# Optimization experiments

Measured on AMD Instinct MI355X. Metric: run time of the kernel, lower is better.

The kernel has to match this reference:

```python
import jax, jax.numpy as jnp
import numpy as np
import math

D_MODEL = 1024
N_HEAD = 16
D_HEAD = D_MODEL // N_HEAD


def setup_inputs() -> dict:
    key = jax.random.key(0)
    k0, k1, k2, k3, k4 = jax.random.split(key, 5)
    B, N = 4, 2048
    inp = jax.random.normal(k0, (B, N, D_MODEL), dtype=jnp.float32)
    # causal mask: True = keep (masked_fill on ~mask)
    mask = jnp.tril(jnp.ones((N, N), dtype=bool))
    # qkv_proj Linear(d_model, 3*d_model); output Linear(d_model, d_model)
    s_in = 1.0 / math.sqrt(D_MODEL)
    W_qkv = jax.random.uniform(k1, (D_MODEL, 3 * D_MODEL), jnp.float32, -s_in, s_in)
    b_qkv = jax.random.uniform(k2, (3 * D_MODEL,), jnp.float32, -s_in, s_in)
    W_out = jax.random.uniform(k3, (D_MODEL, D_MODEL), jnp.float32, -s_in, s_in)
    b_out = jax.random.uniform(k4, (D_MODEL,), jnp.float32, -s_in, s_in)
    return {"input": inp, "W_qkv": W_qkv, "b_qkv": b_qkv,
            "W_out": W_out, "b_out": b_out, "mask": mask}


def reference(input, W_qkv, b_qkv, W_out, b_out, mask):
    B, N, d = input.shape
    qkv = input @ W_qkv + b_qkv                       # [B,N,3d]  (dropout=eval no-op)
    q, k, v = jnp.split(qkv, 3, axis=-1)
    # [B,N,H,Dh] -> [B,H,N,Dh]
    q = q.reshape(B, N, N_HEAD, D_HEAD).transpose(0, 2, 1, 3)
    k = k.reshape(B, N, N_HEAD, D_HEAD).transpose(0, 2, 1, 3)
    v = v.reshape(B, N, N_HEAD, D_HEAD).transpose(0, 2, 1, 3)
    scale = 1.0 / math.sqrt(D_HEAD)
    scores = jnp.einsum('bhqd,bhkd->bhqk', q, k) * scale   # [B,H,N,N]
    scores = jnp.where(mask, scores, -jnp.inf)
    attn = jax.nn.softmax(scores, axis=-1)
    out = jnp.einsum('bhqk,bhkd->bhqd', attn, v)           # [B,H,N,Dh]
    out = out.transpose(0, 2, 1, 3).reshape(B, N, d)       # concat heads
    return out @ W_out + b_out
```

## Files before the change

kernel.cpp:

```cpp
#include <hip/hip_runtime.h>
#include <hip/hip_bf16.h>

typedef unsigned short u16;
typedef unsigned u32;
typedef __attribute__((ext_vector_type(4))) unsigned short u16x4;
typedef __attribute__((ext_vector_type(8))) unsigned short u16x8;
typedef __attribute__((ext_vector_type(4))) unsigned u32x4;
typedef __attribute__((ext_vector_type(8))) __bf16 bf16x8;
typedef __attribute__((ext_vector_type(4))) float f32x4;

typedef __attribute__((address_space(1))) void as1v;
typedef __attribute__((address_space(3))) void as3v;

#define MFMA16(a, b, c) __builtin_amdgcn_mfma_f32_16x16x32_bf16(a, b, c, 0, 0, 0)

__device__ __forceinline__ u16 f2bf(float f) {
    unsigned u = __builtin_bit_cast(unsigned, f);
    u += 0x7fffu + ((u >> 16) & 1u);
    return (u16)(u >> 16);
}

__device__ __forceinline__ u32 pkbf(float lo, float hi) {
    u32 r;
    asm("v_cvt_pk_bf16_f32 %0, %1, %2" : "=v"(r) : "v"(lo), "v"(hi));
    return r;
}

__device__ __forceinline__ void gload16(const void* g, void* l) {
    __builtin_amdgcn_global_load_lds((as1v*)g, (as3v*)l, 16, 0, 0);
}

__global__ void convert_f32_bf16(const float* __restrict__ in, u16* __restrict__ out, int n4) {
    int i = blockIdx.x * blockDim.x + threadIdx.x;
    if (i < n4) {
        float4 v = *(const float4*)&in[(size_t)i * 4];
        u16x4 o;
        o.x = f2bf(v.x); o.y = f2bf(v.y); o.z = f2bf(v.z); o.w = f2bf(v.w);
        *(u16x4*)&out[(size_t)i * 4] = o;
    }
}

__global__ void transpose_convert(const float* __restrict__ in, u16* __restrict__ out, int R, int C) {
    __shared__ float tl[64][65];
    const int rb = blockIdx.x, cb = blockIdx.y;
    const int tid = threadIdx.x;
    for (int it = 0; it < 4; ++it) {
        int lin = (tid + it * 256) * 4;
        int r = lin >> 6, c = lin & 63;
        float4 v = *(const float4*)&in[(size_t)(rb * 64 + r) * C + cb * 64 + c];
        tl[r][c + 0] = v.x; tl[r][c + 1] = v.y; tl[r][c + 2] = v.z; tl[r][c + 3] = v.w;
    }
    __syncthreads();
    for (int it = 0; it < 4; ++it) {
        int lin = (tid + it * 256) * 4;
        int oc = lin >> 6, orr = lin & 63;
        u16x4 o;
        o.x = f2bf(tl[orr + 0][oc]);
        o.y = f2bf(tl[orr + 1][oc]);
        o.z = f2bf(tl[orr + 2][oc]);
        o.w = f2bf(tl[orr + 3][oc]);
        *(u16x4*)&out[(size_t)(cb * 64 + oc) * R + rb * 64 + orr] = o;
    }
}

__global__ void transpose_v(const u16* __restrict__ vbuf, u16* __restrict__ vtb) {
    __shared__ u16 tl[64][65];
    const int nb = blockIdx.x, bh = blockIdx.y;
    const int tid = threadIdx.x;
    for (int it = 0; it < 2; ++it) {
        int lin = (tid + it * 256) * 8;
        int nl = lin >> 6, dh = lin & 63;
        u16x8 v = *(const u16x8*)&vbuf[((size_t)bh * 2048 + nb * 64 + nl) * 64 + dh];
#pragma unroll
        for (int j = 0; j < 8; ++j) tl[dh + j][nl] = v[j];
    }
    __syncthreads();
    for (int it = 0; it < 2; ++it) {
        int lin = (tid + it * 256) * 8;
        int dh = lin >> 6, nl = lin & 63;
        u16x8 o;
#pragma unroll
        for (int j = 0; j < 8; ++j) o[j] = tl[dh][nl + j];
        *(u16x8*)&vtb[((size_t)bh * 64 + dh) * 2048 + nb * 64 + nl] = o;
    }
}

__global__ __launch_bounds__(256) void gemm_bt(
    const u16* __restrict__ A, const u16* __restrict__ Bt, const float* __restrict__ bias,
    int M, int N, int K, int mode,
    u16* __restrict__ qb, u16* __restrict__ kb, u16* __restrict__ vb, float* __restrict__ outf) {
    __shared__ u16 Al[128 * 32];
    __shared__ u16 Bl[128 * 32];
    const int bm = blockIdx.x, bn = blockIdx.y;
    const int tid = threadIdx.x, wid = tid >> 6, lane = tid & 63;
    const int wr = wid >> 1, wc = wid & 1;
    const int l15 = lane & 15, lhi = lane >> 4;

    f32x4 acc[4][4];
#pragma unroll
    for (int i = 0; i < 4; ++i)
#pragma unroll
        for (int j = 0; j < 4; ++j) acc[i][j] = (f32x4){0.f, 0.f, 0.f, 0.f};

    for (int k0 = 0; k0 < K; k0 += 32) {
        __syncthreads();
#pragma unroll
        for (int s = 0; s < 2; ++s) {
            int lin0 = (wid * 2 + s) * 1024;
            int off = lin0 + lane * 16;
            int row = off >> 6, colb = off & 63;
            const u16* ga = A + (size_t)(bm * 128 + row) * K + k0 + (colb >> 1);
            gload16(ga, (char*)Al + lin0);
            const u16* gb = Bt + (size_t)(bn * 128 + row) * K + k0 + (colb >> 1);
            gload16(gb, (char*)Bl + lin0);
        }
        __syncthreads();
        bf16x8 af[4], bfr[4];
#pragma unroll
        for (int mt = 0; mt < 4; ++mt)
            af[mt] = *(const bf16x8*)&Al[(wr * 64 + mt * 16 + l15) * 32 + lhi * 8];
#pragma unroll
        for (int nt = 0; nt < 4; ++nt)
            bfr[nt] = *(const bf16x8*)&Bl[(wc * 64 + nt * 16 + l15) * 32 + lhi * 8];
#pragma unroll
        for (int mt = 0; mt < 4; ++mt)
#pragma unroll
            for (int nt = 0; nt < 4; ++nt)
                acc[mt][nt] = MFMA16(af[mt], bfr[nt], acc[mt][nt]);
    }

#pragma unroll
    for (int mt = 0; mt < 4; ++mt)
#pragma unroll
        for (int nt = 0; nt < 4; ++nt)
#pragma unroll
            for (int v = 0; v < 4; ++v) {
                int rg = bm * 128 + wr * 64 + mt * 16 + lhi * 4 + v;
                int cg = bn * 128 + wc * 64 + nt * 16 + l15;
                float val = acc[mt][nt][v] + bias[cg];
                if (mode == 0) {
                    int which = cg >> 10, rem = cg & 1023;
                    int hh = rem >> 6, dh = rem & 63;
                    int bb = rg >> 11, n = rg & 2047;
                    size_t idx = (((size_t)bb * 16 + hh) * 2048 + n) * 64 + dh;
                    if (which == 0) qb[idx] = f2bf(val * 0.18033688011112042f);
                    else if (which == 1) kb[idx] = f2bf(val);
                    else vb[idx] = f2bf(val);
                } else {
                    outf[(size_t)rg * N + cg] = val;
                }
            }
}

__global__ __launch_bounds__(256, 2) void attn_kernel(
    const u16* __restrict__ qbuf, const u16* __restrict__ kbuf,
    const u16* __restrict__ vtb, u16* __restrict__ obuf) {
    __shared__ u16 Kl[2][64 * 64];
    __shared__ u16 Vl[2][64 * 64];
    const int p = blockIdx.x, bh = blockIdx.y;
    const int b = bh >> 4, h = bh & 15;
    const int tid = threadIdx.x, wid = tid >> 6, lane = tid & 63;
    const int l15 = lane & 15, lhi = lane >> 4;
    const int qA0 = p * 64 + wid * 16;
    const int qB0 = (31 - p) * 64 + wid * 16;
    const int ntA = p + 1;
    const int ntmax = 32 - p;

    bf16x8 qfA[2], qfB[2];
    {
        const u16* qa = qbuf + ((size_t)bh * 2048 + qA0 + l15) * 64 + lhi * 8;
        const u16* qbp = qbuf + ((size_t)bh * 2048 + qB0 + l15) * 64 + lhi * 8;
        qfA[0] = *(const bf16x8*)(qa);
        qfA[1] = *(const bf16x8*)(qa + 32);
        qfB[0] = *(const bf16x8*)(qbp);
        qfB[1] = *(const bf16x8*)(qbp + 32);
    }

    float mA = -1e30f, lA = 0.f, mB = -1e30f, lB = 0.f;
    f32x4 oA[4], oB[4];
#pragma unroll
    for (int d = 0; d < 4; ++d) {
        oA[d] = (f32x4){0.f, 0.f, 0.f, 0.f};
        oB[d] = (f32x4){0.f, 0.f, 0.f, 0.f};
    }

    const int srow = lane >> 3;
    const int scolb = ((lane & 7) * 16) ^ (srow << 4);

    auto stage = [&](int buf, int t) {
        const int kbase = t * 64;
#pragma unroll
        for (int s = 0; s < 2; ++s) {
            int sg = wid * 2 + s;
            int row = sg * 8 + srow;
            const u16* gk = kbuf + ((size_t)bh * 2048 + kbase + row) * 64 + (scolb >> 1);
            gload16(gk, (char*)Kl[buf] + sg * 1024);
            const u16* gv = vtb + ((size_t)bh * 64 + row) * 2048 + kbase + (scolb >> 1);
            gload16(gv, (char*)Vl[buf] + sg * 1024);
        }
    };

    auto computeTile = [&](int bufc, int t, int q0, const bf16x8* qf,
                           float& m, float& l, f32x4* oa) {
        const char* Kb = (const char*)Kl[bufc];
        const char* Vb = (const char*)Vl[bufc];
        f32x4 s[4];
        __builtin_amdgcn_s_setprio(1);
#pragma unroll
        for (int kb4 = 0; kb4 < 4; ++kb4) {
            const int r = kb4 * 16 + l15;
            const int sw = (r & 7) << 4;
            const int rowb = r * 128;
            f32x4 a = (f32x4){0.f, 0.f, 0.f, 0.f};
            a = MFMA16(*(const bf16x8*)(Kb + rowb + ((lhi * 16) ^ sw)), qf[0], a);
            a = MFMA16(*(const bf16x8*)(Kb + rowb + ((64 + lhi * 16) ^ sw)), qf[1], a);
            s[kb4] = a;
        }
        __builtin_amdgcn_s_setprio(0);
        const int qg = q0 + l15;
        if (64 * t + 63 > q0) {
#pragma unroll
            for (int kb4 = 0; kb4 < 4; ++kb4)
#pragma unroll
                for (int v = 0; v < 4; ++v) {
                    int kg = 64 * t + kb4 * 16 + lhi * 4 + v;
                    if (kg > qg) s[kb4][v] = -1e30f;
                }
        }
        float pm = fmaxf(fmaxf(fmaxf(s[0][0], s[0][1]), fmaxf(s[0][2], s[0][3])),
                         fmaxf(fmaxf(s[1][0], s[1][1]), fmaxf(s[1][2], s[1][3])));
        pm = fmaxf(pm, fmaxf(fmaxf(fmaxf(s[2][0], s[2][1]), fmaxf(s[2][2], s[2][3])),
                             fmaxf(fmaxf(s[3][0], s[3][1]), fmaxf(s[3][2], s[3][3]))));
        pm = fmaxf(pm, __shfl_xor(pm, 16, 64));
        pm = fmaxf(pm, __shfl_xor(pm, 32, 64));
        float nm = fmaxf(m, pm);
        float f = exp2f(m - nm);
        m = nm;
        float rs = 0.f;
#pragma unroll
        for (int kb4 = 0; kb4 < 4; ++kb4)
#pragma unroll
            for (int v = 0; v < 4; ++v) {
                float e = exp2f(s[kb4][v] - nm);
                s[kb4][v] = e;
                rs += e;
            }
        rs += __shfl_xor(rs, 16, 64);
        rs += __shfl_xor(rs, 32, 64);
        l = l * f + rs;
#pragma unroll
        for (int d = 0; d < 4; ++d)
#pragma unroll
            for (int v = 0; v < 4; ++v) oa[d][v] *= f;
        u32 pw0[4], pw1[4];
        pw0[0] = pkbf(s[0][0], s[0][1]); pw0[1] = pkbf(s[0][2], s[0][3]);
        pw0[2] = pkbf(s[1][0], s[1][1]); pw0[3] = pkbf(s[1][2], s[1][3]);
        pw1[0] = pkbf(s[2][0], s[2][1]); pw1[1] = pkbf(s[2][2], s[2][3]);
        pw1[2] = pkbf(s[3][0], s[3][1]); pw1[3] = pkbf(s[3][2], s[3][3]);
        __builtin_amdgcn_s_setprio(1);
#pragma unroll
        for (int ks = 0; ks < 2; ++ks) {
            bf16x8 pb = __builtin_bit_cast(bf16x8,
                ks == 0 ? (u32x4){pw0[0], pw0[1], pw0[2], pw0[3]}
                        : (u32x4){pw1[0], pw1[1], pw1[2], pw1[3]});
#pragma unroll
            for (int dhb = 0; dhb < 4; ++dhb) {
                const int r = dhb * 16 + l15;
                const int sw = (r & 7) << 4;
                u16x4 v0 = *(const u16x4*)(Vb + r * 128 + ((ks * 64 + 8 * lhi) ^ sw));
                u16x4 v1 = *(const u16x4*)(Vb + r * 128 + ((ks * 64 + 32 + 8 * lhi) ^ sw));
                u16x8 vv = {v0[0], v0[1], v0[2], v0[3], v1[0], v1[1], v1[2], v1[3]};
                oa[dhb] = MFMA16(__builtin_bit_cast(bf16x8, vv), pb, oa[dhb]);
            }
        }
        __builtin_amdgcn_s_setprio(0);
    };

    stage(0, 0);
    int cur = 0;
    for (int t = 0; t < ntmax; ++t) {
        __syncthreads();
        if (t + 1 < ntmax) stage(cur ^ 1, t + 1);
        computeTile(cur, t, qB0, qfB, mB, lB, oB);
        if (t < ntA) computeTile(cur, t, qA0, qfA, mA, lA, oA);
        cur ^= 1;
    }

    auto epi = [&](int q0, float l, const f32x4* oa) {
        const float rl = 1.f / l;
        const int q = q0 + l15;
        const size_t rowoff = ((size_t)b * 2048 + q) * 1024 + h * 64;
#pragma unroll
        for (int dhb = 0; dhb < 4; ++dhb) {
            u16x4 w;
#pragma unroll
            for (int v = 0; v < 4; ++v) w[v] = f2bf(oa[dhb][v] * rl);
            *(u16x4*)&obuf[rowoff + dhb * 16 + lhi * 4] = w;
        }
    };
    epi(qA0, lA, oA);
    epi(qB0, lB, oB);
}

extern "C" void kernel_launch(void* const* d_in, const int* in_sizes, int n_in,
                              void* d_out, int out_size, void* d_ws, size_t ws_size,
                              hipStream_t stream) {
    const float* inp   = (const float*)d_in[0];
    const float* W_qkv = (const float*)d_in[1];
    const float* b_qkv = (const float*)d_in[2];
    const float* W_out = (const float*)d_in[3];
    const float* b_out = (const float*)d_in[4];
    float* out = (float*)d_out;

    u16* xb   = (u16*)d_ws;
    u16* wqt  = xb + 8388608;
    u16* wot  = wqt + 3145728;
    u16* qbuf = wot + 1048576;
    u16* kbuf = qbuf + 8388608;
    u16* vbuf = kbuf + 8388608;
    u16* vtb  = vbuf + 8388608;
    u16* obuf = vtb + 8388608;

    convert_f32_bf16<<<8192, 256, 0, stream>>>(inp, xb, 2097152);
    transpose_convert<<<dim3(16, 48), 256, 0, stream>>>(W_qkv, wqt, 1024, 3072);
    transpose_convert<<<dim3(16, 16), 256, 0, stream>>>(W_out, wot, 1024, 1024);
    gemm_bt<<<dim3(64, 24), 256, 0, stream>>>(xb, wqt, b_qkv, 8192, 3072, 1024, 0,
                                              qbuf, kbuf, vbuf, nullptr);
    transpose_v<<<dim3(32, 64), 256, 0, stream>>>(vbuf, vtb);
    attn_kernel<<<dim3(16, 64), 256, 0, stream>>>(qbuf, kbuf, vtb, obuf);
    gemm_bt<<<dim3(64, 8), 256, 0, stream>>>(obuf, wot, b_out, 8192, 1024, 1024, 1,
                                             nullptr, nullptr, nullptr, out);
}
```

Before: 219.1 us.

## Replace QKV projection GEMM with 256x256-tile pipelined kernel

New measurement: 206.5 us. 5.7% less time.

```diff
diff --git a/kernel.cpp b/kernel.cpp
--- a/kernel.cpp
+++ b/kernel.cpp
@@ -82,6 +82,132 @@
 #pragma unroll
         for (int j = 0; j < 8; ++j) o[j] = tl[dh][nl + j];
         *(u16x8*)&vtb[((size_t)bh * 64 + dh) * 2048 + nb * 64 + nl] = o;
+    }
+}
+
+__global__ __launch_bounds__(512, 2) void gemm256_qkv(
+    const u16* __restrict__ A, const u16* __restrict__ Bt, const float* __restrict__ bias,
+    u16* __restrict__ qb, u16* __restrict__ kb, u16* __restrict__ vb) {
+    constexpr int K = 1024;
+    constexpr int NT = 32;
+    __shared__ u16 ldsu[65536];
+
+    const int bid = blockIdx.x;
+    const int swz = (bid & 7) * 48 + (bid >> 3);
+    const int bm = swz / 12, bn = swz % 12;
+
+    const int tid = threadIdx.x, wid = tid >> 6, lane = tid & 63;
+    const int wr = wid >> 2, wc = wid & 3;
+    const int l15 = lane & 15, lhi = lane >> 4;
+
+    const int sslot = (lane & 7) ^ (lane >> 3);
+    const int kcol = (sslot & 3) * 8;
+    const int mloc = (lane >> 3) * 2 + (sslot >> 2);
+
+    const u16* Arow[2];
+    const u16* Brow[2];
+#pragma unroll
+    for (int li = 0; li < 2; ++li) {
+        int sg = wid * 2 + li;
+        int m = sg * 16 + mloc;
+        Arow[li] = A + (size_t)(bm * 256 + m) * K + kcol;
+        Brow[li] = Bt + (size_t)(bn * 256 + m) * K + kcol;
+    }
+
+    auto stageA = [&](int buf, int t) {
+#pragma unroll
+        for (int li = 0; li < 2; ++li) {
+            int sg = wid * 2 + li;
+            gload16(Arow[li] + t * 32, (char*)ldsu + buf * 32768 + sg * 1024);
+        }
+    };
+    auto stageB = [&](int buf, int t) {
+#pragma unroll
+        for (int li = 0; li < 2; ++li) {
+            int sg = wid * 2 + li;
+            gload16(Brow[li] + t * 32, (char*)ldsu + buf * 32768 + 16384 + sg * 1024);
+        }
+    };
+
+    const int rslot = ((l15 & 1) * 4 + lhi) ^ ((l15 >> 1) & 7);
+    const int fragoff = (l15 >> 1) * 64 + rslot * 8;
+
+    f32x4 acc[8][4];
+#pragma unroll
+    for (int i = 0; i < 8; ++i)
+#pragma unroll
+        for (int j = 0; j < 4; ++j) acc[i][j] = (f32x4){0.f, 0.f, 0.f, 0.f};
+
+    auto doTile = [&](int cur, int tstage, bool dostage) {
+        const u16* Ab = ldsu + cur * 16384 + wr * 4096 + fragoff;
+        const u16* Bb = ldsu + cur * 16384 + 8192 + wc * 2048 + fragoff;
+        bf16x8 af[8], b0, b1;
+#pragma unroll
+        for (int mf = 0; mf < 8; ++mf) af[mf] = *(const bf16x8*)(Ab + mf * 512);
+        b0 = *(const bf16x8*)(Bb);
+        b1 = *(const bf16x8*)(Bb + 512);
+        if (dostage) stageA(tstage & 3, tstage);
+        __builtin_amdgcn_s_setprio(1);
+#pragma unroll
+        for (int mf = 0; mf < 8; ++mf) {
+            acc[mf][0] = MFMA16(af[mf], b0, acc[mf][0]);
+            acc[mf][1] = MFMA16(af[mf], b1, acc[mf][1]);
+        }
+        __builtin_amdgcn_s_setprio(0);
+        b0 = *(const bf16x8*)(Bb + 1024);
+        b1 = *(const bf16x8*)(Bb + 1536);
+        if (dostage) stageB(tstage & 3, tstage);
+        __builtin_amdgcn_s_setprio(1);
+#pragma unroll
+        for (int mf = 0; mf < 8; ++mf) {
+            acc[mf][2] = MFMA16(af[mf], b0, acc[mf][2]);
+            acc[mf][3] = MFMA16(af[mf], b1, acc[mf][3]);
+        }
+        __builtin_amdgcn_s_setprio(0);
+    };
+
+    stageA(0, 0); stageB(0, 0);
+    stageA(1, 1); stageB(1, 1);
+    stageA(2, 2); stageB(2, 2);
+    asm volatile("s_waitcnt vmcnt(8)" ::: "memory");
+    __builtin_amdgcn_s_barrier();
+    __builtin_amdgcn_sched_barrier(0);
+
+    for (int t = 0; t < NT - 3; ++t) {
+        doTile(t & 3, t + 3, true);
+        asm volatile("s_waitcnt vmcnt(8)" ::: "memory");
+        __builtin_amdgcn_s_barrier();
+        __builtin_amdgcn_sched_barrier(0);
+    }
+    doTile((NT - 3) & 3, 0, false);
+    asm volatile("s_waitcnt vmcnt(4)" ::: "memory");
+    __builtin_amdgcn_s_barrier();
+    __builtin_amdgcn_sched_barrier(0);
+    doTile((NT - 2) & 3, 0, false);
+    asm volatile("s_waitcnt vmcnt(0)" ::: "memory");
+    __builtin_amdgcn_s_barrier();
+    __builtin_amdgcn_sched_barrier(0);
+    doTile((NT - 1) & 3, 0, false);
+
+    const int bnbase = bn * 256 + wc * 64;
+#pragma unroll
+    for (int nf = 0; nf < 4; ++nf) {
+        int cg = bnbase + nf * 16 + l15;
+        float bv = bias[cg];
+        int which = cg >> 10, rem = cg & 1023;
+        u16* dst = (which == 0) ? qb : (which == 1) ? kb : vb;
+        float qs = (which == 0) ? 0.18033688011112042f : 1.0f;
+        size_t colterm = (size_t)(rem >> 6) * 131072 + (size_t)(rem & 63);
+#pragma unroll
+        for (int mf = 0; mf < 8; ++mf) {
+            int rgb = bm * 256 + wr * 128 + mf * 16 + lhi * 4;
+            size_t rowterm = (size_t)(rgb >> 11) * 2097152 + (size_t)(rgb & 2047) * 64;
+#pragma unroll
+            for (int v = 0; v < 4; ++v) {
+                float val = (acc[mf][nf][v] + bv) * qs;
+                dst[rowterm + (size_t)v * 64 + colterm] = f2bf(val);
+            }
+        }
     }
 }
 
@@ -324,8 +450,7 @@
     convert_f32_bf16<<<8192, 256, 0, stream>>>(inp, xb, 2097152);
     transpose_convert<<<dim3(16, 48), 256, 0, stream>>>(W_qkv, wqt, 1024, 3072);
     transpose_convert<<<dim3(16, 16), 256, 0, stream>>>(W_out, wot, 1024, 1024);
-    gemm_bt<<<dim3(64, 24), 256, 0, stream>>>(xb, wqt, b_qkv, 8192, 3072, 1024, 0,
-                                              qbuf, kbuf, vbuf, nullptr);
+    gemm256_qkv<<<384, 512, 0, stream>>>(xb, wqt, b_qkv, qbuf, kbuf, vbuf);
     transpose_v<<<dim3(32, 64), 256, 0, stream>>>(vbuf, vtb);
     attn_kernel<<<dim3(16, 64), 256, 0, stream>>>(qbuf, kbuf, vtb, obuf);
     gemm_bt<<<dim3(64, 8), 256, 0, stream>>>(obuf, wot, b_out, 8192, 1024, 1024, 1,
```
